# Optimization experiments

Hardware: AMD Instinct MI355X
Metric: run time of the kernel (lower is better)

Reference implementation:

```python
import jax, jax.numpy as jnp
import numpy as np

N = 100000    # nodes
E = 800000    # directed edges
EF = 16       # edge features
NF = 1        # node features (forced by the module's MLP-size constraint)
HID = NF * 8  # NNConv out = 8
H1, C1 = 8, 16  # gat1 heads / per-head channels -> 128
NC = 16       # num_classes (gat2: heads=1, out=NC)


def setup_inputs() -> dict:
    key = jax.random.key(0)
    ks = jax.random.split(key, 20)
    s = 0.1
    return {
        "x": jax.random.normal(ks[0], (N, NF), jnp.float32),
        "edge_index": jax.random.randint(ks[1], (2, E), 0, N, jnp.int64),
        "edge_attr": jax.random.normal(ks[2], (E, EF), jnp.float32),
        # edge MLP: Linear(EF,8) -> ReLU -> Linear(8,8)
        "w1": jax.random.normal(ks[3], (EF, HID), jnp.float32) * s,
        "b1": jnp.zeros((HID,), jnp.float32),
        "w2": jax.random.normal(ks[4], (HID, HID), jnp.float32) * s,
        "b2": jnp.zeros((HID,), jnp.float32),
        # NNConv root weight + bias
        "root": jax.random.normal(ks[5], (NF, HID), jnp.float32) * s,
        "nn_bias": jnp.zeros((HID,), jnp.float32),
        # GAT1: in 8 -> 16 ch x 8 heads
        "g1W": jax.random.normal(ks[6], (HID, H1 * C1), jnp.float32) * s,
        "g1as": jax.random.normal(ks[7], (H1, C1), jnp.float32) * s,
        "g1ad": jax.random.normal(ks[8], (H1, C1), jnp.float32) * s,
        "g1b": jnp.zeros((H1 * C1,), jnp.float32),
        # GAT2: in 128 -> NC, 1 head
        "g2W": jax.random.normal(ks[9], (H1 * C1, NC), jnp.float32) * s,
        "g2as": jax.random.normal(ks[10], (1, NC), jnp.float32) * s,
        "g2ad": jax.random.normal(ks[11], (1, NC), jnp.float32) * s,
        "g2b": jnp.zeros((NC,), jnp.float32),
    }


def _gat(h_in, W, a_src, a_dst, bias, src, dst, n, heads, ch):
    # h: [N, heads, ch]
    h = (h_in @ W).reshape(n, heads, ch)
    e_s = jnp.einsum("nhc,hc->nh", h, a_src)   # per-node src logits
    e_d = jnp.einsum("nhc,hc->nh", h, a_dst)
    e = jax.nn.leaky_relu(e_s[src] + e_d[dst], 0.2)      # [E2, heads]
    m = jax.ops.segment_max(e, dst, num_segments=n)      # segment softmax
    e = jnp.exp(e - m[dst])
    z = jax.ops.segment_sum(e, dst, num_segments=n)
    alpha = e / (z[dst] + 1e-16)                          # [E2, heads]
    out = jax.ops.segment_sum(alpha[:, :, None] * h[src], dst, num_segments=n)
    return out.reshape(n, heads * ch) + bias


def reference(x, edge_index, edge_attr, w1, b1, w2, b2, root, nn_bias,
              g1W, g1as, g1ad, g1b, g2W, g2as, g2ad, g2b):
    n = x.shape[0]
    src, dst = edge_index[0], edge_index[1]

    # ---- NNConv (aggr='mean'): per-edge weight from edge MLP ----
    w_e = jax.nn.relu(edge_attr @ w1 + b1) @ w2 + b2      # [E, NF*HID]
    w_e = w_e.reshape(-1, NF, HID)
    msg = jnp.einsum("ei,eio->eo", x[src], w_e)            # [E, HID]
    sums = jax.ops.segment_sum(msg, dst, num_segments=n)
    cnt = jax.ops.segment_sum(jnp.ones((msg.shape[0],), msg.dtype), dst, num_segments=n)
    aggr = sums / jnp.maximum(cnt, 1.0)[:, None]
    h = jax.nn.relu(aggr + x @ root + nn_bias)             # [N, 8]
    # dropout: eval mode -> identity

    # ---- add self-loops (PyG GATConv default) ----
    loops = jnp.arange(n, dtype=src.dtype)
    src2 = jnp.concatenate([src, loops])
    dst2 = jnp.concatenate([dst, loops])

    h = jax.nn.elu(_gat(h, g1W, g1as, g1ad, g1b, src2, dst2, n, H1, C1))  # [N,128]
    out = _gat(h, g2W, g2as, g2ad, g2b, src2, dst2, n, 1, NC)             # [N,16]
    return jax.nn.log_softmax(out, axis=1)
```

## Files before the change

kernel.cpp:

```cpp
#include <hip/hip_runtime.h>
#include <hip/hip_fp16.h>
#include <math.h>

constexpr int NN  = 100000;
constexpr int NE  = 800000;
constexpr int H1 = 8, C1 = 16;
constexpr int D1 = H1 * C1;
constexpr int NC = 16;
constexpr int CAP = 40;
constexpr float LOG2E = 1.44269504f;

static inline int cdiv(int a, int b) { return (a + b - 1) / b; }

typedef int   v4i __attribute__((ext_vector_type(4)));
typedef float v2f __attribute__((ext_vector_type(2)));

__device__ inline __half2 h2_bits(unsigned u) {
    __half2 r; __builtin_memcpy(&r, &u, 4); return r;
}
__device__ inline __half2 shflx_h2(__half2 v, int off) {
    int iv; __builtin_memcpy(&iv, &v, 4);
    iv = __shfl_xor(iv, off);
    __half2 r; __builtin_memcpy(&r, &iv, 4); return r;
}

__global__ void fill_cur(int* __restrict__ cur) {
    int i = blockIdx.x * blockDim.x + threadIdx.x;
    if (i < NN) cur[i] = i * CAP;
}

__global__ void nnconv_scatter(const float* __restrict__ x,
                               const int* __restrict__ src, const int* __restrict__ dst,
                               const float* __restrict__ ea,
                               const float* __restrict__ w1, const float* __restrict__ b1,
                               const float* __restrict__ w2, const float* __restrict__ b2,
                               int* __restrict__ cursor,
                               int* __restrict__ src_s, __half* __restrict__ msg_s) {
    __shared__ float sw1[16 * 8], sw2[8 * 8], sb1[8], sb2[8];
    int t = threadIdx.x;
    if (t < 128) sw1[t] = w1[t];
    else if (t < 192) sw2[t - 128] = w2[t - 128];
    else if (t < 200) sb1[t - 192] = b1[t - 192];
    else if (t < 208) sb2[t - 200] = b2[t - 200];
    __syncthreads();
    int e = blockIdx.x * blockDim.x + t;
    if (e >= NE) return;

    float a[16];
    const float4* ea4 = (const float4*)(ea + (size_t)e * 16);
    float4 v0 = ea4[0], v1 = ea4[1], v2 = ea4[2], v3 = ea4[3];
    a[0]=v0.x; a[1]=v0.y; a[2]=v0.z; a[3]=v0.w;
    a[4]=v1.x; a[5]=v1.y; a[6]=v1.z; a[7]=v1.w;
    a[8]=v2.x; a[9]=v2.y; a[10]=v2.z; a[11]=v2.w;
    a[12]=v3.x; a[13]=v3.y; a[14]=v3.z; a[15]=v3.w;

    float hdn[8];
#pragma unroll
    for (int j = 0; j < 8; j++) {
        float s = sb1[j];
#pragma unroll
        for (int i = 0; i < 16; i++) s = fmaf(a[i], sw1[i * 8 + j], s);
        hdn[j] = fmaxf(s, 0.f);
    }
    int sn = src[e], dn = dst[e];
    float xv = x[sn];
    __align__(16) __half msg[8];
#pragma unroll
    for (int j = 0; j < 8; j++) {
        float s = sb2[j];
#pragma unroll
        for (int i = 0; i < 8; i++) s = fmaf(hdn[i], sw2[i * 8 + j], s);
        msg[j] = __float2half(xv * s);
    }
    int pos = atomicAdd(&cursor[dn], 1);
    if (pos < dn * CAP + CAP) {
        v4i mv; __builtin_memcpy(&mv, msg, 16);
        __builtin_nontemporal_store(mv, (v4i*)(msg_s + (unsigned)pos * 8u));
        src_s[pos] = sn;
    }
}

__global__ void fused_node1(const float* __restrict__ x,
                            const int* __restrict__ cur,
                            const __half* __restrict__ msg_s,
                            const float* __restrict__ root, const float* __restrict__ nb,
                            const float* __restrict__ W,
                            const float* __restrict__ as_, const float* __restrict__ ad_,
                            unsigned char* __restrict__ h1f8,
                            float* __restrict__ es, float* __restrict__ ed) {
    int t = blockIdx.x * blockDim.x + threadIdx.x;
    if (t >= NN * 8) return;
    int n = t >> 3, j = t & 7;
    int rs = n * CAP;
    int d = min(cur[n] - rs, CAP);

    float p0 = 0.f, p1 = 0.f, p2 = 0.f, p3 = 0.f;
    float p4 = 0.f, p5 = 0.f, p6 = 0.f, p7 = 0.f;
    for (int k = j; k < d; k += 8) {
        uint4 m = *(const uint4*)(msg_s + (unsigned)(rs + k) * 8u);
        float2 f0 = __half22float2(h2_bits(m.x));
        float2 f1 = __half22float2(h2_bits(m.y));
        float2 f2 = __half22float2(h2_bits(m.z));
        float2 f3 = __half22float2(h2_bits(m.w));
        p0 += f0.x; p1 += f0.y; p2 += f1.x; p3 += f1.y;
        p4 += f2.x; p5 += f2.y; p6 += f3.x; p7 += f3.y;
    }
    float k0 = (j & 4) ? p4 : p0, s0 = (j & 4) ? p0 : p4;
    float k1 = (j & 4) ? p5 : p1, s1 = (j & 4) ? p1 : p5;
    float k2 = (j & 4) ? p6 : p2, s2 = (j & 4) ? p2 : p6;
    float k3 = (j & 4) ? p7 : p3, s3 = (j & 4) ? p3 : p7;
    k0 += __shfl_xor(s0, 4); k1 += __shfl_xor(s1, 4);
    k2 += __shfl_xor(s2, 4); k3 += __shfl_xor(s3, 4);
    float m0 = (j & 2) ? k2 : k0, n0 = (j & 2) ? k0 : k2;
    float m1 = (j & 2) ? k3 : k1, n1 = (j & 2) ? k1 : k3;
    m0 += __shfl_xor(n0, 2); m1 += __shfl_xor(n1, 2);
    float q  = (j & 1) ? m1 : m0, r = (j & 1) ? m0 : m1;
    float sum = q + __shfl_xor(r, 1);

    float hj = fmaxf(sum / fmaxf((float)d, 1.f) + x[n] * root[j] + nb[j], 0.f);

    float hv[8];
#pragma unroll
    for (int k = 0; k < 8; k++) hv[k] = __shfl(hj, k, 8);

    int hd = j;
    float acc[16];
#pragma unroll
    for (int c = 0; c < 16; c++) acc[c] = 0.f;
#pragma unroll
    for (int k = 0; k < 8; k++) {
        const float* wr = W + k * D1 + hd * 16;
#pragma unroll
        for (int c = 0; c < 16; c++) acc[c] = fmaf(hv[k], wr[c], acc[c]);
    }
    float s = 0.f, dd = 0.f;
#pragma unroll
    for (int c = 0; c < 16; c++) {
        s = fmaf(acc[c], as_[hd * 16 + c], s);
        dd = fmaf(acc[c], ad_[hd * 16 + c], dd);
    }
    v4i pk;
#pragma unroll
    for (int w = 0; w < 4; w++) {
        int wd = __builtin_amdgcn_cvt_pk_fp8_f32(acc[4*w] * 16.f, acc[4*w+1] * 16.f, 0, false);
        wd = __builtin_amdgcn_cvt_pk_fp8_f32(acc[4*w+2] * 16.f, acc[4*w+3] * 16.f, wd, true);
        pk[w] = wd;
    }
    *(v4i*)(h1f8 + (unsigned)n * 128u + hd * 16) = pk;
    es[t] = s * LOG2E;
    ed[t] = dd * LOG2E;
}

__global__ __launch_bounds__(256) void gat1_gather(
        const int* __restrict__ cur,
        const int* __restrict__ src_s,
        const float* __restrict__ es, const float* __restrict__ ed,
        const unsigned char* __restrict__ h1f8, const float* __restrict__ b,
        const float* __restrict__ W2,
        const float* __restrict__ as2, const float* __restrict__ ad2,
        __half* __restrict__ h2h, float* __restrict__ es2, float* __restrict__ ed2) {
    __shared__ float sW2[2048];
    __shared__ float so[4][4][132];
    int tid = threadIdx.x;
    for (int idx = tid; idx < 2048; idx += 256) sW2[idx] = W2[idx];
    __syncthreads();

    int wv = tid >> 6, lane = tid & 63;
    int g  = lane >> 4;
    int cl = lane & 15;
    int hd = cl >> 1;
    float4 bv0 = *((const float4*)(b + cl * 8));
    float4 bv1 = *((const float4*)(b + cl * 8 + 4));

    int base = (blockIdx.x * 4 + wv) * 4;
    for (int i = 0; i < 4; i++) {
        int node = base + i;
        int rs = node * CAP;
        int d = min(cur[node] - rs, CAP);
        const int* sp = src_s + rs;
        float edn = ed[(unsigned)node * 8u + hd];

        float vs = es[(unsigned)node * 8u + hd] + edn;
        vs = fmaxf(vs, 0.2f * vs);
        float a0 = (g == 0) ? __builtin_amdgcn_exp2f(vs) : 0.f;
        float z = a0;
        uint2 gl = *(const uint2*)(h1f8 + (unsigned)node * 128u + cl * 8);
        v2f d0 = __builtin_amdgcn_cvt_pk_f32_fp8(gl.x, false);
        v2f d1 = __builtin_amdgcn_cvt_pk_f32_fp8(gl.x, true);
        v2f d2 = __builtin_amdgcn_cvt_pk_f32_fp8(gl.y, false);
        v2f d3 = __builtin_amdgcn_cvt_pk_f32_fp8(gl.y, true);
        float c0 = a0 * d0[0], c1 = a0 * d0[1], c2 = a0 * d1[0], c3 = a0 * d1[1];
        float c4 = a0 * d2[0], c5 = a0 * d2[1], c6 = a0 * d3[0], c7 = a0 * d3[1];

        for (int k = g; k < d; k += 4) {
            int s = sp[k];
            float v = es[(unsigned)s * 8u + hd] + edn;
            v = fmaxf(v, 0.2f * v);
            float a = __builtin_amdgcn_exp2f(v);
            uint2 ge = *(const uint2*)(h1f8 + (unsigned)s * 128u + cl * 8);
            v2f e0 = __builtin_amdgcn_cvt_pk_f32_fp8(ge.x, false);
            v2f e1 = __builtin_amdgcn_cvt_pk_f32_fp8(ge.x, true);
            v2f e2 = __builtin_amdgcn_cvt_pk_f32_fp8(ge.y, false);
            v2f e3 = __builtin_amdgcn_cvt_pk_f32_fp8(ge.y, true);
            z += a;
            c0 = fmaf(a, e0[0], c0); c1 = fmaf(a, e0[1], c1);
            c2 = fmaf(a, e1[0], c2); c3 = fmaf(a, e1[1], c3);
            c4 = fmaf(a, e2[0], c4); c5 = fmaf(a, e2[1], c5);
            c6 = fmaf(a, e3[0], c6); c7 = fmaf(a, e3[1], c7);
        }
        z += __shfl_xor(z, 16); z += __shfl_xor(z, 32);
        c0 += __shfl_xor(c0, 16); c0 += __shfl_xor(c0, 32);
        c1 += __shfl_xor(c1, 16); c1 += __shfl_xor(c1, 32);
        c2 += __shfl_xor(c2, 16); c2 += __shfl_xor(c2, 32);
        c3 += __shfl_xor(c3, 16); c3 += __shfl_xor(c3, 32);
        c4 += __shfl_xor(c4, 16); c4 += __shfl_xor(c4, 32);
        c5 += __shfl_xor(c5, 16); c5 += __shfl_xor(c5, 32);
        c6 += __shfl_xor(c6, 16); c6 += __shfl_xor(c6, 32);
        c7 += __shfl_xor(c7, 16); c7 += __shfl_xor(c7, 32);

        float rz = 1.f / (16.f * (z + 1e-16f));
        float o0 = fmaf(c0, rz, bv0.x), o1 = fmaf(c1, rz, bv0.y);
        float o2 = fmaf(c2, rz, bv0.z), o3 = fmaf(c3, rz, bv0.w);
        float o4 = fmaf(c4, rz, bv1.x), o5 = fmaf(c5, rz, bv1.y);
        float o6 = fmaf(c6, rz, bv1.z), o7 = fmaf(c7, rz, bv1.w);
        o0 = o0 > 0.f ? o0 : __expf(o0) - 1.f;
        o1 = o1 > 0.f ? o1 : __expf(o1) - 1.f;
        o2 = o2 > 0.f ? o2 : __expf(o2) - 1.f;
        o3 = o3 > 0.f ? o3 : __expf(o3) - 1.f;
        o4 = o4 > 0.f ? o4 : __expf(o4) - 1.f;
        o5 = o5 > 0.f ? o5 : __expf(o5) - 1.f;
        o6 = o6 > 0.f ? o6 : __expf(o6) - 1.f;
        o7 = o7 > 0.f ? o7 : __expf(o7) - 1.f;
        if (g == 0) {
            float4* sp2 = (float4*)&so[wv][i][cl * 8];
            sp2[0] = make_float4(o0, o1, o2, o3);
            sp2[1] = make_float4(o4, o5, o6, o7);
        }
    }
    __asm__ __volatile__("s_waitcnt lgkmcnt(0)" ::: "memory");

    int nl = lane >> 4, c = lane & 15;
    float partial = 0.f;
#pragma unroll 4
    for (int k = 0; k < 128; k += 2) {
        float2 sv = *(const float2*)&so[wv][nl][k];
        partial = fmaf(sv.x, sW2[k * 16 + c], partial);
        partial = fmaf(sv.y, sW2[(k + 1) * 16 + c], partial);
    }
    float ta = partial * as2[c], tb = partial * ad2[c];
#pragma unroll
    for (int off = 1; off < 16; off <<= 1) {
        ta += __shfl_xor(ta, off);
        tb += __shfl_xor(tb, off);
    }
    h2h[(unsigned)(base + nl) * 16u + c] = __float2half(partial);
    if (c == 0) {
        es2[base + nl] = ta * LOG2E;
        ed2[base + nl] = tb * LOG2E;
    }
}

__global__ __launch_bounds__(256) void gat2_gather(
        const int* __restrict__ cur,
        const int* __restrict__ src_s,
        const float* __restrict__ es, const float* __restrict__ ed,
        const __half* __restrict__ h2h, const float* __restrict__ b,
        float* __restrict__ out) {
    int tid = threadIdx.x;
    int wv = tid >> 6, lane = tid & 63;
    int g = lane >> 3, l = lane & 7;
    const unsigned* h2i = (const unsigned*)h2h;
    float2 bv = ((const float2*)b)[l];
    int base = (blockIdx.x * 4 + wv) * 4;
    for (int i = 0; i < 4; i++) {
        int node = base + i;
        int rs = node * CAP;
        int d = min(cur[node] - rs, CAP);
        const int* sp = src_s + rs;
        float edn = ed[node];
        float vs = es[node] + edn;
        vs = fmaxf(vs, 0.2f * vs);
        float a0 = (g == 0) ? __builtin_amdgcn_exp2f(vs) : 0.f;
        float z = a0;
        __half2 acc = __hmul2(__float2half2_rn(a0),
                              h2_bits(h2i[(unsigned)node * 8u + l]));

        for (int k = g; k < d; k += 8) {
            int s = sp[k];
            float v = es[s] + edn;
            v = fmaxf(v, 0.2f * v);
            float a = __builtin_amdgcn_exp2f(v);
            unsigned hraw = h2i[(unsigned)s * 8u + l];
            z += a;
            acc = __hfma2(__float2half2_rn(a), h2_bits(hraw), acc);
        }
        z += __shfl_xor(z, 8); z += __shfl_xor(z, 16); z += __shfl_xor(z, 32);
        acc = __hadd2(acc, shflx_h2(acc, 8));
        acc = __hadd2(acc, shflx_h2(acc, 16));
        acc = __hadd2(acc, shflx_h2(acc, 32));

        float rz = 1.f / (z + 1e-16f);
        float2 f = __half22float2(acc);
        float o0 = fmaf(f.x, rz, bv.x);
        float o1 = fmaf(f.y, rz, bv.y);
        float mx = fmaxf(o0, o1);
        mx = fmaxf(mx, __shfl_xor(mx, 1));
        mx = fmaxf(mx, __shfl_xor(mx, 2));
        mx = fmaxf(mx, __shfl_xor(mx, 4));
        float ss = __expf(o0 - mx) + __expf(o1 - mx);
        ss += __shfl_xor(ss, 1); ss += __shfl_xor(ss, 2); ss += __shfl_xor(ss, 4);
        float lg = mx + __logf(ss);
        if (g == 0)
            ((float2*)out)[(unsigned)node * 8u + l] = make_float2(o0 - lg, o1 - lg);
    }
}

extern "C" void kernel_launch(void* const* d_in, const int* in_sizes, int n_in,
                              void* d_out, int out_size, void* d_ws, size_t ws_size,
                              hipStream_t stream) {
    const float* x    = (const float*)d_in[0];
    const int*   ei   = (const int*)d_in[1];
    const float* ea   = (const float*)d_in[2];
    const float* w1   = (const float*)d_in[3];
    const float* b1   = (const float*)d_in[4];
    const float* w2   = (const float*)d_in[5];
    const float* b2   = (const float*)d_in[6];
    const float* root = (const float*)d_in[7];
    const float* nb   = (const float*)d_in[8];
    const float* g1W  = (const float*)d_in[9];
    const float* g1as = (const float*)d_in[10];
    const float* g1ad = (const float*)d_in[11];
    const float* g1b  = (const float*)d_in[12];
    const float* g2W  = (const float*)d_in[13];
    const float* g2as = (const float*)d_in[14];
    const float* g2ad = (const float*)d_in[15];
    const float* g2b  = (const float*)d_in[16];
    float* out = (float*)d_out;

    const int* src = ei;
    const int* dst = ei + NE;

    float* ws = (float*)d_ws;
    size_t o = 0;
    __half* msg_s  = (__half*)(ws + o); o += (size_t)NN * CAP * 4;
    unsigned char* h1f8 = (unsigned char*)(ws + o); o += (size_t)NN * 32;
    __half* h2h    = (__half*)(ws + o); o += (size_t)NN * NC / 2;
    int*  src_s = (int*)(ws + o); o += (size_t)NN * CAP;
    int*  cur   = (int*)(ws + o); o += NN;
    float* es1  = ws + o; o += (size_t)NN * H1;
    float* ed1  = ws + o; o += (size_t)NN * H1;
    float* es2  = ws + o; o += NN;
    float* ed2  = ws + o; o += NN;
    (void)ws_size; (void)in_sizes; (void)n_in; (void)out_size;

    const int B = 256;

    fill_cur<<<cdiv(NN, B), B, 0, stream>>>(cur);

    nnconv_scatter<<<cdiv(NE, B), B, 0, stream>>>(x, src, dst, ea, w1, b1, w2, b2,
                                                  cur, src_s, msg_s);
    fused_node1<<<cdiv(NN * 8, B), B, 0, stream>>>(x, cur, msg_s, root, nb,
                                                   g1W, g1as, g1ad, h1f8, es1, ed1);
    gat1_gather<<<NN / 16, B, 0, stream>>>(cur, src_s, es1, ed1, h1f8,
                                           g1b, g2W, g2as, g2ad, h2h, es2, ed2);
    gat2_gather<<<NN / 16, B, 0, stream>>>(cur, src_s, es2, ed2, h2h, g2b, out);
}
```

Baseline: 298.7 us.

## Accumulate NNConv messages with packed fp16 atomics instead of bucketed message storage

The edge kernel no longer writes each fp16 message into a per-destination bucket. It atomically adds the messages into a per-node fp16 sum buffer using packed half2 atomics, and the init kernel now zeroes that buffer. The node kernel then reads one sum per channel instead of gathering and reducing up to CAP messages. This removes a large scatter write and a gather read, in exchange for contended fp16 atomics, accumulation in fp16 that may lose precision, and nondeterministic summation order.

```diff
diff --git a/kernel.cpp b/kernel.cpp
--- a/kernel.cpp
+++ b/kernel.cpp
@@ -24,9 +24,13 @@
     __half2 r; __builtin_memcpy(&r, &iv, 4); return r;
 }
 
-__global__ void fill_cur(int* __restrict__ cur) {
+__global__ void init_kernel(int* __restrict__ cur, __half* __restrict__ sums) {
     int i = blockIdx.x * blockDim.x + threadIdx.x;
-    if (i < NN) cur[i] = i * CAP;
+    if (i < NN) {
+        cur[i] = i * CAP;
+        v4i z = {0, 0, 0, 0};
+        *(v4i*)(sums + (unsigned)i * 8u) = z;
+    }
 }
 
 __global__ void nnconv_scatter(const float* __restrict__ x,
@@ -35,7 +39,7 @@
                                const float* __restrict__ w1, const float* __restrict__ b1,
                                const float* __restrict__ w2, const float* __restrict__ b2,
                                int* __restrict__ cursor,
-                               int* __restrict__ src_s, __half* __restrict__ msg_s) {
+                               int* __restrict__ src_s, __half* __restrict__ sums) {
     __shared__ float sw1[16 * 8], sw2[8 * 8], sb1[8], sb2[8];
     int t = threadIdx.x;
     if (t < 128) sw1[t] = w1[t];
@@ -64,25 +68,25 @@
     }
     int sn = src[e], dn = dst[e];
     float xv = x[sn];
-    __align__(16) __half msg[8];
+    float msg[8];
 #pragma unroll
     for (int j = 0; j < 8; j++) {
         float s = sb2[j];
 #pragma unroll
         for (int i = 0; i < 8; i++) s = fmaf(hdn[i], sw2[i * 8 + j], s);
-        msg[j] = __float2half(xv * s);
-    }
+        msg[j] = xv * s;
+    }
+    __half2* sp = (__half2*)(sums + (unsigned)dn * 8u);
+#pragma unroll
+    for (int w = 0; w < 4; w++)
+        unsafeAtomicAdd(sp + w, __floats2half2_rn(msg[2 * w], msg[2 * w + 1]));
     int pos = atomicAdd(&cursor[dn], 1);
-    if (pos < dn * CAP + CAP) {
-        v4i mv; __builtin_memcpy(&mv, msg, 16);
-        __builtin_nontemporal_store(mv, (v4i*)(msg_s + (unsigned)pos * 8u));
-        src_s[pos] = sn;
-    }
+    if (pos < dn * CAP + CAP) src_s[pos] = sn;
 }
 
 __global__ void fused_node1(const float* __restrict__ x,
                             const int* __restrict__ cur,
-                            const __half* __restrict__ msg_s,
+                            const __half* __restrict__ sums,
                             const float* __restrict__ root, const float* __restrict__ nb,
                             const float* __restrict__ W,
                             const float* __restrict__ as_, const float* __restrict__ ad_,
@@ -91,33 +95,10 @@
     int t = blockIdx.x * blockDim.x + threadIdx.x;
     if (t >= NN * 8) return;
     int n = t >> 3, j = t & 7;
-    int rs = n * CAP;
-    int d = min(cur[n] - rs, CAP);
-
-    float p0 = 0.f, p1 = 0.f, p2 = 0.f, p3 = 0.f;
-    float p4 = 0.f, p5 = 0.f, p6 = 0.f, p7 = 0.f;
-    for (int k = j; k < d; k += 8) {
-        uint4 m = *(const uint4*)(msg_s + (unsigned)(rs + k) * 8u);
-        float2 f0 = __half22float2(h2_bits(m.x));
-        float2 f1 = __half22float2(h2_bits(m.y));
-        float2 f2 = __half22float2(h2_bits(m.z));
-        float2 f3 = __half22float2(h2_bits(m.w));
-        p0 += f0.x; p1 += f0.y; p2 += f1.x; p3 += f1.y;
-        p4 += f2.x; p5 += f2.y; p6 += f3.x; p7 += f3.y;
-    }
-    float k0 = (j & 4) ? p4 : p0, s0 = (j & 4) ? p0 : p4;
-    float k1 = (j & 4) ? p5 : p1, s1 = (j & 4) ? p1 : p5;
-    float k2 = (j & 4) ? p6 : p2, s2 = (j & 4) ? p2 : p6;
-    float k3 = (j & 4) ? p7 : p3, s3 = (j & 4) ? p3 : p7;
-    k0 += __shfl_xor(s0, 4); k1 += __shfl_xor(s1, 4);
-    k2 += __shfl_xor(s2, 4); k3 += __shfl_xor(s3, 4);
-    float m0 = (j & 2) ? k2 : k0, n0 = (j & 2) ? k0 : k2;
-    float m1 = (j & 2) ? k3 : k1, n1 = (j & 2) ? k1 : k3;
-    m0 += __shfl_xor(n0, 2); m1 += __shfl_xor(n1, 2);
-    float q  = (j & 1) ? m1 : m0, r = (j & 1) ? m0 : m1;
-    float sum = q + __shfl_xor(r, 1);
-
-    float hj = fmaxf(sum / fmaxf((float)d, 1.f) + x[n] * root[j] + nb[j], 0.f);
+    int dtrue = cur[n] - n * CAP;
+
+    float sum = __half2float(sums[(unsigned)n * 8u + j]);
+    float hj = fmaxf(sum / fmaxf((float)dtrue, 1.f) + x[n] * root[j] + nb[j], 0.f);
 
     float hv[8];
 #pragma unroll
@@ -342,7 +323,7 @@
 
     float* ws = (float*)d_ws;
     size_t o = 0;
-    __half* msg_s  = (__half*)(ws + o); o += (size_t)NN * CAP * 4;
+    __half* sums   = (__half*)(ws + o); o += (size_t)NN * 4;
     unsigned char* h1f8 = (unsigned char*)(ws + o); o += (size_t)NN * 32;
     __half* h2h    = (__half*)(ws + o); o += (size_t)NN * NC / 2;
     int*  src_s = (int*)(ws + o); o += (size_t)NN * CAP;
@@ -355,11 +336,11 @@
 
     const int B = 256;
 
-    fill_cur<<<cdiv(NN, B), B, 0, stream>>>(cur);
+    init_kernel<<<cdiv(NN, B), B, 0, stream>>>(cur, sums);
 
     nnconv_scatter<<<cdiv(NE, B), B, 0, stream>>>(x, src, dst, ea, w1, b1, w2, b2,
-                                                  cur, src_s, msg_s);
-    fused_node1<<<cdiv(NN * 8, B), B, 0, stream>>>(x, cur, msg_s, root, nb,
+                                                  cur, src_s, sums);
+    fused_node1<<<cdiv(NN * 8, B), B, 0, stream>>>(x, cur, sums, root, nb,
                                                    g1W, g1as, g1ad, h1f8, es1, ed1);
     gat1_gather<<<NN / 16, B, 0, stream>>>(cur, src_s, es1, ed1, h1f8,
                                            g1b, g2W, g2as, g2ad, h2h, es2, ed2);
```

Result: slower. 434.5 us (+45.4%).
